# Kernel tuning notes

Hardware: AMD Instinct MI355X
Metric: run time of the kernel (lower is better)

## Reference

```python
import jax, jax.numpy as jnp
import numpy as np

MODES1 = 20
MODES2 = 20
WIDTH = 64
NUM_LAYERS = 4
B, H, W = 8, 256, 256


def _conv2d(x, w, b, pad):
    # x: (B,C,H,W), w: (O,I,kh,kw)
    y = jax.lax.conv_general_dilated(
        x, w, window_strides=(1, 1), padding=[(pad, pad), (pad, pad)],
        dimension_numbers=('NCHW', 'OIHW', 'NCHW'))
    return y + b[None, :, None, None]


def _spectral_conv(x, w1, w2, m1, m2):
    # x: (B,C,H,W); w1,w2: (I,O,m1,m2,2) real/imag pairs
    h, w = x.shape[-2], x.shape[-1]
    x_ft = jnp.fft.rfft2(x, norm='ortho')              # (B,C,H,W//2+1) complex
    w1c = w1[..., 0] + 1j * w1[..., 1]
    w2c = w2[..., 0] + 1j * w2[..., 1]
    top = jnp.einsum('bixy,ioxy->boxy', x_ft[:, :, :m1, :m2], w1c)
    bot = jnp.einsum('bixy,ioxy->boxy', x_ft[:, :, -m1:, :m2], w2c)
    out_ft = jnp.zeros((x.shape[0], w1.shape[1], h, w // 2 + 1), dtype=x_ft.dtype)
    out_ft = out_ft.at[:, :, :m1, :m2].set(top)
    out_ft = out_ft.at[:, :, -m1:, :m2].set(bot)
    return jnp.fft.irfft2(out_ft, s=(h, w), norm='ortho')


def setup_inputs() -> dict:
    key = jax.random.key(0)
    ks = jax.random.split(key, 16)
    C = WIDTH
    L = NUM_LAYERS
    scale = 1.0 / (C * C)
    inp = {
        'x': jax.random.normal(ks[0], (B, H, W, 3), dtype=jnp.float32),
        'fc0_w': jax.random.normal(ks[1], (3, C), dtype=jnp.float32) * 0.1,
        'fc0_b': jnp.zeros((C,), dtype=jnp.float32),
        'w1': scale * jax.random.uniform(ks[2], (L, C, C, MODES1, MODES2, 2), dtype=jnp.float32),
        'w2': scale * jax.random.uniform(ks[3], (L, C, C, MODES1, MODES2, 2), dtype=jnp.float32),
        'convh_w': jax.random.normal(ks[4], (L, C, C, 3, 3), dtype=jnp.float32) * 0.02,
        'convh_b': jnp.zeros((L, C), dtype=jnp.float32),
        'convw_w': jax.random.normal(ks[5], (L, C, C, 3, 3), dtype=jnp.float32) * 0.02,
        'convw_b': jnp.zeros((L, C), dtype=jnp.float32),
        'pw_w': jax.random.normal(ks[6], (L, C, C, 1, 1), dtype=jnp.float32) * 0.05,
        'pw_b': jnp.zeros((L, C), dtype=jnp.float32),
        'fc1_w': jax.random.normal(ks[7], (C, 128), dtype=jnp.float32) * 0.05,
        'fc1_b': jnp.zeros((128,), dtype=jnp.float32),
        'fc2_w': jax.random.normal(ks[8], (128, 1), dtype=jnp.float32) * 0.05,
        'fc2_b': jnp.zeros((1,), dtype=jnp.float32),
    }
    return inp


def reference(x, fc0_w, fc0_b, w1, w2, convh_w, convh_b, convw_w, convw_b,
              pw_w, pw_b, fc1_w, fc1_b, fc2_w, fc2_b):
    # fc0 lift: (B,H,W,3) -> (B,H,W,C) -> (B,C,H,W)
    h = jnp.einsum('bhwc,cd->bhwd', x, fc0_w) + fc0_b
    h = jnp.transpose(h, (0, 3, 1, 2))
    for i in range(NUM_LAYERS):
        x1 = _spectral_conv(h, w1[i], w2[i], MODES1, MODES2)
        # Mamba fallback block: two 3x3 convs summed (LayerNorm unused in forward)
        x2 = _conv2d(h, convh_w[i], convh_b[i], 1) + _conv2d(h, convw_w[i], convw_b[i], 1)
        x3 = _conv2d(h, pw_w[i], pw_b[i], 0)
        h = x1 + x2 + x3
        if i < NUM_LAYERS - 1:
            h = jax.nn.gelu(h, approximate=False)
    h = jnp.transpose(h, (0, 2, 3, 1))                  # (B,H,W,C)
    h = jnp.einsum('bhwc,cd->bhwd', h, fc1_w) + fc1_b
    h = jax.nn.gelu(h, approximate=False)
    out = jnp.einsum('bhwc,cd->bhwd', h, fc2_w) + fc2_b  # (B,H,W,1)
    return out
```

## Files before the change

kernel.cpp:

```cpp
#include <hip/hip_runtime.h>
#include <math.h>

#define NB 8
#define NC 64
#define NH 256
#define NW 256
#define NM 40
#define NKX 20
#define NL 4

typedef _Float16 f16x8 __attribute__((ext_vector_type(8)));
typedef float    f32x4 __attribute__((ext_vector_type(4)));

#define PERCB_FLOATS ((size_t)(2*4194304 + 655360 + 2*102400))
#define FIXED_FLOATS ((size_t)(6553600 + 10240 + 20480 + 147456 + 256 + 155648))

static __device__ __forceinline__ float gelu_f(float v) {
  return 0.5f * v * (1.f + erff(v * 0.70710678118654752f));
}
static __device__ __forceinline__ unsigned pack2(_Float16 a, _Float16 b) {
  union { _Float16 h[2]; unsigned u; } x; x.h[0] = a; x.h[1] = b; return x.u;
}

__global__ __launch_bounds__(256) void k_tables(float2* __restrict__ Tx,
                                                float2* __restrict__ Ty) {
  int t = blockIdx.x * 256 + threadIdx.x;
  const float w = (float)(2.0 * 3.14159265358979323846 / 256.0);
  if (t < NKX * 256) {
    int kx = t >> 8, x = t & 255;
    float th = (float)((kx * x) & 255) * w;
    Tx[t] = make_float2(cosf(th), sinf(th));
  }
  int u = t - NKX * 256;
  if (u >= 0 && u < NM * 256) {
    int m = u >> 8, y = u & 255;
    int ky = (m < 20) ? m : (m + 216);
    float th = (float)((ky * y) & 255) * w;
    Ty[u] = make_float2(cosf(th), sinf(th));
  }
}

__global__ __launch_bounds__(256) void k_wc(const float* __restrict__ ch,
                                            const float* __restrict__ cw,
                                            const float* __restrict__ pw,
                                            const float* __restrict__ chb,
                                            const float* __restrict__ cwb,
                                            const float* __restrict__ pwb,
                                            float* __restrict__ wc,
                                            float* __restrict__ bc) {
  int t = blockIdx.x * 256 + threadIdx.x;
  if (t < NL * NC * NC * 9) {
    int tap = t % 9;
    int io  = t / 9;
    int o   = io % 64;
    int i   = (io / 64) % 64;
    int l   = io / 4096;
    int src = ((l * 64 + o) * 64 + i) * 9 + tap;
    float v = ch[src] + cw[src];
    if (tap == 4) v += pw[(l * 64 + o) * 64 + i];
    wc[t] = v;
  }
  if (t < NL * NC) bc[t] = chb[t] + cwb[t] + pwb[t];
}

__global__ __launch_bounds__(256) void k_wpack(const float* __restrict__ wc,
                                               _Float16* __restrict__ whi,
                                               _Float16* __restrict__ wlo) {
  int t = blockIdx.x * 256 + threadIdx.x;
  int lane = t & 63;
  int nt   = (t >> 6) & 3;
  int chunk = (t >> 8) % 18;
  int l4   = t / 4608;
  int tap = chunk >> 1, half = chunk & 1;
  int o = nt * 16 + (lane & 15);
  _Float16 hi[8], lo[8];
  #pragma unroll
  for (int j = 0; j < 8; ++j) {
    int i = half * 32 + ((lane >> 4) << 3) + j;
    float v = wc[((l4 * 64 + i) * 64 + o) * 9 + tap];
    _Float16 h = (_Float16)v;
    hi[j] = h;
    lo[j] = (_Float16)(v - (float)h);
  }
  *(f16x8*)(whi + (size_t)t * 8) = *(f16x8*)hi;
  *(f16x8*)(wlo + (size_t)t * 8) = *(f16x8*)lo;
}

__global__ __launch_bounds__(256) void k_hpack(const float* __restrict__ w1,
                                               _Float16* __restrict__ whi,
                                               _Float16* __restrict__ wlo) {
  int t = blockIdx.x * 256 + threadIdx.x;
  int lane = t & 63;
  int nt   = (t >> 6) & 7;
  int chunk = t >> 9;
  int jo = nt * 16 + (lane & 15);
  _Float16 hi[8], lo[8];
  #pragma unroll
  for (int j = 0; j < 8; ++j) {
    int c = chunk * 32 + ((lane >> 4) << 3) + j;
    float v = w1[c * 128 + jo];
    _Float16 h = (_Float16)v;
    hi[j] = h;
    lo[j] = (_Float16)(v - (float)h);
  }
  *(f16x8*)(whi + (size_t)t * 8) = *(f16x8*)hi;
  *(f16x8*)(wlo + (size_t)t * 8) = *(f16x8*)lo;
}

__global__ __launch_bounds__(256) void k_fc0(const float* __restrict__ x,
                                             const float* __restrict__ w,
                                             const float* __restrict__ b,
                                             float* __restrict__ h, int b0) {
  int t = blockIdx.x * 256 + threadIdx.x;
  int ch = t & 63;
  int px = t >> 6;
  const float* xp = x + ((size_t)b0 * 65536 + px) * 3;
  h[t] = xp[0] * w[ch] + xp[1] * w[64 + ch] + xp[2] * w[128 + ch] + b[ch];
}

__global__ __launch_bounds__(256) void k_fwdx(const float* __restrict__ h,
                                              const float2* __restrict__ Tx,
                                              float2* __restrict__ Fx) {
  __shared__ float sm[16384];
  int bidx = blockIdx.x;
  int y  = bidx & 255;
  int bb = bidx >> 8;
  const float* hp = h + ((size_t)bb * 65536 + y * 256) * 64;
  for (int e = threadIdx.x; e < 4096; e += 256)
    *(float4*)(sm + e * 4) = *(const float4*)(hp + e * 4);
  __syncthreads();
  int w  = threadIdx.x >> 6;
  int ch = threadIdx.x & 63;
  float ar[5] = {0,0,0,0,0}, ai[5] = {0,0,0,0,0};
  #pragma unroll 4
  for (int x = 0; x < 256; x += 2) {
    float v0 = sm[x * 64 + ch];
    float v1 = sm[x * 64 + 64 + ch];
    #pragma unroll
    for (int q = 0; q < 5; ++q) {
      int kx = w * 5 + q;
      float4 t4 = *(const float4*)(Tx + kx * 256 + x);
      ar[q] += v0 * t4.x + v1 * t4.z;
      ai[q] -= v0 * t4.y + v1 * t4.w;
    }
  }
  float2* fp = Fx + ((size_t)(bb * 64 + ch) * 256 + y) * 20;
  #pragma unroll
  for (int q = 0; q < 5; ++q) fp[w * 5 + q] = make_float2(ar[q], ai[q]);
}

__global__ __launch_bounds__(256) void k_fwdy(const float2* __restrict__ Fx,
                                              const float2* __restrict__ Ty,
                                              float2* __restrict__ FxyT, int nbc) {
  __shared__ float2 sFx[5120];
  int bc = blockIdx.x;
  const float4* src = (const float4*)(Fx + (size_t)bc * 5120);
  float4* dst = (float4*)sFx;
  for (int e = threadIdx.x; e < 2560; e += 256) dst[e] = src[e];
  __syncthreads();
  for (int mk = threadIdx.x; mk < 800; mk += 256) {
    int kx = mk % 20, m = mk / 20;
    const float2* tp = Ty + m * 256;
    float re = 0.f, im = 0.f;
    #pragma unroll 4
    for (int yy = 0; yy < 256; ++yy) {
      float2 f = sFx[yy * 20 + kx];
      float2 wv = tp[yy];
      re += f.x * wv.x + f.y * wv.y;
      im += f.y * wv.x - f.x * wv.y;
    }
    FxyT[(size_t)mk * nbc + bc] = make_float2(re * (1.f / 256.f), im * (1.f / 256.f));
  }
}

__global__ __launch_bounds__(256) void k_wT(const float* __restrict__ w1,
                                            const float* __restrict__ w2,
                                            float2* __restrict__ wT, int l) {
  __shared__ float2 tile[32][33];
  int mk0 = blockIdx.x * 32;
  int io0 = blockIdx.y * 32;
  int tx = threadIdx.x & 31, ty0 = threadIdx.x >> 5;
  #pragma unroll
  for (int s = 0; s < 4; ++s) {
    int ty = ty0 * 4 + s;
    int mk = mk0 + tx, io = io0 + ty;
    int m = mk / 20, kx = mk % 20;
    const float* src = (m < 20) ? w1 : w2;
    int mm = (m < 20) ? m : (m - 20);
    size_t idx = ((((size_t)l * 4096 + io) * 20 + mm) * 20 + kx) * 2;
    tile[ty][tx] = make_float2(src[idx], src[idx + 1]);
  }
  __syncthreads();
  #pragma unroll
  for (int s = 0; s < 4; ++s) {
    int ty = ty0 * 4 + s;
    wT[(size_t)(mk0 + ty) * 4096 + (io0 + tx)] = tile[tx][ty];
  }
}

__global__ __launch_bounds__(256) void k_mix(const float2* __restrict__ FxyT,
                                             const float2* __restrict__ wT,
                                             float2* __restrict__ G, int nrows) {
  __shared__ float2 sf[512];
  int mk = blockIdx.x;
  for (int t = threadIdx.x; t < nrows; t += 256)
    sf[t] = FxyT[(size_t)mk * nrows + t];
  __syncthreads();
  const float2* wp = wT + (size_t)mk * 4096;
  for (int t = threadIdx.x; t < nrows; t += 256) {
    int b = t >> 6, o = t & 63;
    const float2* fb = sf + b * 64;
    float re = 0.f, im = 0.f;
    #pragma unroll 8
    for (int i = 0; i < 64; ++i) {
      float2 f = fb[i];
      float2 w = wp[i * 64 + o];
      re += f.x * w.x - f.y * w.y;
      im += f.x * w.y + f.y * w.x;
    }
    G[(size_t)(b * 64 + o) * 800 + mk] = make_float2(re, im);
  }
}

__global__ __launch_bounds__(256) void k_invy(const float2* __restrict__ G,
                                              const float2* __restrict__ Ty,
                                              float2* __restrict__ Gy) {
  int t  = blockIdx.x * 256 + threadIdx.x;
  int kx = t % 20;
  int y  = (t / 20) & 255;
  int bc = t / 5120;
  const float2* gp = G + (size_t)bc * 800 + kx;
  float re = 0.f, im = 0.f;
  #pragma unroll 4
  for (int m = 0; m < 40; ++m) {
    float2 g = gp[m * 20];
    float2 w = Ty[m * 256 + y];
    re += g.x * w.x - g.y * w.y;
    im += g.x * w.y + g.y * w.x;
  }
  Gy[t] = make_float2(re, im);
}

__global__ __launch_bounds__(256, 3) void k_conv(const float* __restrict__ hin,
                                                 const f16x8* __restrict__ wph,
                                                 const f16x8* __restrict__ wpl,
                                                 const float* __restrict__ bcb,
                                                 const float2* __restrict__ Gy,
                                                 const float2* __restrict__ Tx,
                                                 float* __restrict__ hout,
                                                 int dogelu) {
  __shared__ unsigned sAu[13056];
  int bidx = blockIdx.x;
  int xt = bidx & 7;
  int yt = (bidx >> 3) & 63;
  int bb = bidx >> 9;
  int x0 = xt << 5, y0 = yt << 2;
  int tid = threadIdx.x;
  int w = tid >> 6, lane = tid & 63, quad = lane >> 4, l15 = lane & 15;

  for (int e = tid; e < 204 * 32; e += 256) {
    int px = e >> 5, chp = e & 31;
    int rg = px / 34, cg = px % 34;
    int gy = y0 - 1 + rg, gx = x0 - 1 + cg;
    float2 v = make_float2(0.f, 0.f);
    if (gy >= 0 && gy < 256 && gx >= 0 && gx < 256)
      v = *(const float2*)(hin + (((size_t)bb * 256 + gy) * 256 + gx) * 64 + chp * 2);
    _Float16 h0 = (_Float16)v.x, h1 = (_Float16)v.y;
    _Float16 l0 = (_Float16)(v.x - (float)h0), l1 = (_Float16)(v.y - (float)h1);
    int dw = (px << 5) + (chp ^ ((px & 7) << 2));
    sAu[dw] = pack2(h0, h1);
    sAu[6528 + dw] = pack2(l0, l1);
  }
  __syncthreads();

  f32x4 acc[2][4];
  #pragma unroll
  for (int s = 0; s < 2; ++s)
    #pragma unroll
    for (int nt = 0; nt < 4; ++nt) acc[s][nt] = (f32x4){0.f, 0.f, 0.f, 0.f};

  #pragma unroll 1
  for (int tap = 0; tap < 9; ++tap) {
    int dy = tap / 3, dx = tap % 3;
    #pragma unroll
    for (int half = 0; half < 2; ++half) {
      int chunk = tap * 2 + half;
      const f16x8* bh = wph + (size_t)(chunk * 4) * 64 + lane;
      const f16x8* bl = wpl + (size_t)(chunk * 4) * 64 + lane;
      f16x8 bfh[4], bfl[4];
      #pragma unroll
      for (int nt = 0; nt < 4; ++nt) { bfh[nt] = bh[nt * 64]; bfl[nt] = bl[nt * 64]; }
      f16x8 afh[2], afl[2];
      #pragma unroll
      for (int s = 0; s < 2; ++s) {
        int px = (w + dy) * 34 + (s * 16 + dx) + l15;
        int dw = (px << 5) + (((half << 4) + (quad << 2)) ^ ((px & 7) << 2));
        afh[s] = *(const f16x8*)(sAu + dw);
        afl[s] = *(const f16x8*)(sAu + 6528 + dw);
      }
      #pragma unroll
      for (int s = 0; s < 2; ++s)
        #pragma unroll
        for (int nt = 0; nt < 4; ++nt) {
          acc[s][nt] = __builtin_amdgcn_mfma_f32_16x16x32_f16(afh[s], bfh[nt], acc[s][nt], 0, 0, 0);
          acc[s][nt] = __builtin_amdgcn_mfma_f32_16x16x32_f16(afh[s], bfl[nt], acc[s][nt], 0, 0, 0);
          acc[s][nt] = __builtin_amdgcn_mfma_f32_16x16x32_f16(afl[s], bfh[nt], acc[s][nt], 0, 0, 0);
        }
    }
  }

  __syncthreads();
  float2* sT  = (float2*)sAu;
  float2* sGy = (float2*)(sAu + 1280);
  float*  sTr = (float*)(sAu + 6528);
  for (int e = tid; e < 640; e += 256) {
    int kx = e >> 5, col = e & 31;
    sT[e] = Tx[kx * 256 + x0 + col];
  }
  const float scale = 1.f / 256.f;
  #pragma unroll 1
  for (int oh = 0; oh < 2; ++oh) {
    __syncthreads();
    for (int e = tid; e < 2560; e += 256) {
      int ol = e / 80, rem = e % 80;
      int row = rem / 20, kx = rem % 20;
      sGy[ol * 82 + row * 20 + kx] =
          Gy[((size_t)(bb * 64 + oh * 32 + ol) * 256 + (y0 + row)) * 20 + kx];
    }
    __syncthreads();
    #pragma unroll
    for (int nt2 = 0; nt2 < 2; ++nt2) {
      int nt = oh * 2 + nt2;
      int ol = nt2 * 16 + l15;
      int o  = oh * 32 + ol;
      float bias = bcb[o];
      const float2* gp = sGy + ol * 82 + w * 20;
      #pragma unroll
      for (int s = 0; s < 2; ++s) {
        int colb = s * 16 + (quad << 2);
        f32x4 sr = {0.f, 0.f, 0.f, 0.f};
        #pragma unroll
        for (int p = 0; p < 10; ++p) {
          float4 g = *(const float4*)(gp + 2 * p);
          float f0 = (p == 0) ? 1.f : 2.f;
          float4 tA = *(const float4*)(sT + (2 * p) * 32 + colb);
          float4 tB = *(const float4*)(sT + (2 * p) * 32 + colb + 2);
          sr.x += f0 * (g.x * tA.x - g.y * tA.y);
          sr.y += f0 * (g.x * tA.z - g.y * tA.w);
          sr.z += f0 * (g.x * tB.x - g.y * tB.y);
          sr.w += f0 * (g.x * tB.z - g.y * tB.w);
          float4 tC = *(const float4*)(sT + (2 * p + 1) * 32 + colb);
          float4 tD = *(const float4*)(sT + (2 * p + 1) * 32 + colb + 2);
          sr.x += 2.f * (g.z * tC.x - g.w * tC.y);
          sr.y += 2.f * (g.z * tC.z - g.w * tC.w);
          sr.z += 2.f * (g.z * tD.x - g.w * tD.y);
          sr.w += 2.f * (g.z * tD.z - g.w * tD.w);
        }
        #pragma unroll
        for (int r = 0; r < 4; ++r) {
          float v = acc[s][nt][r] + bias + sr[r] * scale;
          if (dogelu) v = gelu_f(v);
          sTr[(w * 32 + s * 16 + (quad << 2) + r) * 36 + ol] = v;
        }
      }
    }
    __syncthreads();
    #pragma unroll
    for (int k = 0; k < 4; ++k) {
      int e = tid + k * 256;
      int P = e >> 3, sub = e & 7;
      float4 v4 = *(const float4*)(sTr + P * 36 + sub * 4);
      int row = P >> 5, px32 = P & 31;
      *(float4*)(hout + (((size_t)bb * 256 + (y0 + row)) * 256 + x0 + px32) * 64
                 + oh * 32 + sub * 4) = v4;
    }
  }
}

__global__ __launch_bounds__(256, 2) void k_head(const float* __restrict__ h,
                                                 const f16x8* __restrict__ whi,
                                                 const f16x8* __restrict__ wlo,
                                                 const float* __restrict__ b1,
                                                 const float* __restrict__ w2,
                                                 const float* __restrict__ b2,
                                                 float* __restrict__ out, int b0) {
  int tid = threadIdx.x;
  int w = tid >> 6, lane = tid & 63, quad = lane >> 4, l15 = lane & 15;
  int px0 = blockIdx.x * 64 + w * 16;

  f32x4 acc[8];
  #pragma unroll
  for (int nt = 0; nt < 8; ++nt) acc[nt] = (f32x4){0.f, 0.f, 0.f, 0.f};

  #pragma unroll
  for (int half = 0; half < 2; ++half) {
    const float* ap = h + (size_t)(px0 + l15) * 64 + half * 32 + quad * 8;
    float4 a0 = *(const float4*)ap;
    float4 a1 = *(const float4*)(ap + 4);
    _Float16 ah[8], al[8];
    float av[8] = {a0.x, a0.y, a0.z, a0.w, a1.x, a1.y, a1.z, a1.w};
    #pragma unroll
    for (int j = 0; j < 8; ++j) {
      ah[j] = (_Float16)av[j];
      al[j] = (_Float16)(av[j] - (float)ah[j]);
    }
    f16x8 afh = *(f16x8*)ah, afl = *(f16x8*)al;
    #pragma unroll
    for (int nt = 0; nt < 8; ++nt) {
      f16x8 bh = whi[(size_t)(half * 8 + nt) * 64 + lane];
      f16x8 bl = wlo[(size_t)(half * 8 + nt) * 64 + lane];
      acc[nt] = __builtin_amdgcn_mfma_f32_16x16x32_f16(afh, bh, acc[nt], 0, 0, 0);
      acc[nt] = __builtin_amdgcn_mfma_f32_16x16x32_f16(afh, bl, acc[nt], 0, 0, 0);
      acc[nt] = __builtin_amdgcn_mfma_f32_16x16x32_f16(afl, bh, acc[nt], 0, 0, 0);
    }
  }

  float part[4] = {0.f, 0.f, 0.f, 0.f};
  #pragma unroll
  for (int nt = 0; nt < 8; ++nt) {
    int jo = nt * 16 + l15;
    float bb1 = b1[jo], ww2 = w2[jo];
    #pragma unroll
    for (int r = 0; r < 4; ++r)
      part[r] += gelu_f(acc[nt][r] + bb1) * ww2;
  }
  #pragma unroll
  for (int r = 0; r < 4; ++r) {
    float v = part[r];
    v += __shfl_xor(v, 1);
    v += __shfl_xor(v, 2);
    v += __shfl_xor(v, 4);
    v += __shfl_xor(v, 8);
    if (l15 == 0)
      out[(size_t)b0 * 65536 + px0 + quad * 4 + r] = v + b2[0];
  }
}

extern "C" void kernel_launch(void* const* d_in, const int* in_sizes, int n_in,
                              void* d_out, int out_size, void* d_ws, size_t ws_size,
                              hipStream_t stream) {
  const float* x    = (const float*)d_in[0];
  const float* fc0w = (const float*)d_in[1];
  const float* fc0b = (const float*)d_in[2];
  const float* w1   = (const float*)d_in[3];
  const float* w2   = (const float*)d_in[4];
  const float* chw  = (const float*)d_in[5];
  const float* chb  = (const float*)d_in[6];
  const float* cww  = (const float*)d_in[7];
  const float* cwb  = (const float*)d_in[8];
  const float* pww  = (const float*)d_in[9];
  const float* pwb  = (const float*)d_in[10];
  const float* fc1w = (const float*)d_in[11];
  const float* fc1b = (const float*)d_in[12];
  const float* fc2w = (const float*)d_in[13];
  const float* fc2b = (const float*)d_in[14];

  int cb = 1;
  for (int cand = 8; cand >= 1; cand >>= 1) {
    size_t need = (PERCB_FLOATS * (size_t)cand + FIXED_FLOATS) * sizeof(float);
    if (ws_size >= need) { cb = cand; break; }
  }

  const size_t szH = (size_t)cb * 4194304;

  float*  ws  = (float*)d_ws;
  float*  h   = ws;
  float*  h2  = h + szH;
  float2* Fx  = (float2*)(h2 + szH);
  float2* Fxy = (float2*)((float*)Fx + (size_t)cb * 655360);
  float2* G   = (float2*)((float*)Fxy + (size_t)cb * 102400);
  float2* wT  = (float2*)((float*)G + (size_t)cb * 102400);
  float2* Tx  = (float2*)((float*)wT + 6553600);
  float2* Ty  = (float2*)((float*)Tx + 10240);
  float*  wcb = (float*)Ty + 20480;
  float*  bcb = wcb + 147456;
  _Float16* wpkhi = (_Float16*)(bcb + 256);
  _Float16* wpklo = wpkhi + 147456;
  _Float16* w1hi  = wpklo + 147456;
  _Float16* w1lo  = w1hi + 8192;
  float2* Gy = Fx;

  k_tables<<<60, 256, 0, stream>>>(Tx, Ty);
  k_wc<<<576, 256, 0, stream>>>(chw, cww, pww, chb, cwb, pwb, wcb, bcb);
  k_wpack<<<72, 256, 0, stream>>>(wcb, wpkhi, wpklo);
  k_hpack<<<4, 256, 0, stream>>>(fc1w, w1hi, w1lo);

  for (int b0 = 0; b0 < NB; b0 += cb) {
    k_fc0<<<cb * 16384, 256, 0, stream>>>(x, fc0w, fc0b, h, b0);
    float* cur = h;
    float* nxt = h2;
    int nbc = cb * 64;
    for (int l = 0; l < NL; ++l) {
      k_fwdx<<<cb * 256, 256, 0, stream>>>(cur, Tx, Fx);
      k_fwdy<<<nbc, 256, 0, stream>>>(Fx, Ty, Fxy, nbc);
      k_wT<<<dim3(25, 128), 256, 0, stream>>>(w1, w2, wT, l);
      k_mix<<<NM * NKX, 256, 0, stream>>>(Fxy, wT, G, nbc);
      k_invy<<<cb * 1280, 256, 0, stream>>>(G, Ty, Gy);
      k_conv<<<cb * 512, 256, 0, stream>>>(cur,
                                           (const f16x8*)(wpkhi + (size_t)l * 36864),
                                           (const f16x8*)(wpklo + (size_t)l * 36864),
                                           bcb + (size_t)l * 64, Gy, Tx, nxt,
                                           (l < NL - 1) ? 1 : 0);
      float* tmp = cur; cur = nxt; nxt = tmp;
    }
    k_head<<<cb * 1024, 256, 0, stream>>>(cur, (const f16x8*)w1hi, (const f16x8*)w1lo,
                                          fc1b, fc2w, fc2b, (float*)d_out, b0);
  }
}
```

Measured before the change: 4.770 ms.

## Compute forward x-DFT with split-fp16 MFMA and simplify conv epilogue stores

The forward x-direction partial DFT is recast as a matrix multiply. Input rows are converted to hi/lo fp16 pairs in shared memory, and a prepacked fp16 twiddle matrix (built once by a new k_txpack kernel) feeds 16x16x32 MFMAs using three-product split precision. This replaces the scalar FMA loop over 256 x positions. The conv epilogue now loads all 64 output channels of Gy at once, hoists the bias loads, and writes results directly to global memory instead of transposing through shared memory in two halves. The direct stores are narrower and less coalesced, and the split-fp16 DFT may differ slightly in accuracy.

After: 4.374 ms. -8.3%, faster.

```diff
diff --git a/kernel.cpp b/kernel.cpp
--- a/kernel.cpp
+++ b/kernel.cpp
@@ -13,7 +13,7 @@
 typedef float    f32x4 __attribute__((ext_vector_type(4)));
 
 #define PERCB_FLOATS ((size_t)(2*4194304 + 655360 + 2*102400))
-#define FIXED_FLOATS ((size_t)(6553600 + 10240 + 20480 + 147456 + 256 + 155648))
+#define FIXED_FLOATS ((size_t)(6553600 + 10240 + 20480 + 147456 + 256 + 167936 + 2048))
 
 static __device__ __forceinline__ float gelu_f(float v) {
   return 0.5f * v * (1.f + erff(v * 0.70710678118654752f));
@@ -38,6 +38,26 @@
     float th = (float)((ky * y) & 255) * w;
     Ty[u] = make_float2(cosf(th), sinf(th));
   }
+}
+
+__global__ __launch_bounds__(256) void k_txpack(_Float16* __restrict__ th,
+                                                _Float16* __restrict__ tl) {
+  int t = blockIdx.x * 256 + threadIdx.x;
+  int j = t & 7, lane = (t >> 3) & 63;
+  int rest = t >> 9;
+  int nt = rest % 3, kc = rest / 3;
+  int x = kc * 32 + ((lane >> 4) << 3) + j;
+  int n = nt * 16 + (lane & 15);
+  float val = 0.f;
+  if (n < 40) {
+    int kx = n >> 1;
+    const float w = (float)(2.0 * 3.14159265358979323846 / 256.0);
+    float ang = (float)((kx * x) & 255) * w;
+    val = (n & 1) ? -sinf(ang) : cosf(ang);
+  }
+  _Float16 hi = (_Float16)val;
+  th[t] = hi;
+  tl[t] = (_Float16)(val - (float)hi);
 }
 
 __global__ __launch_bounds__(256) void k_wc(const float* __restrict__ ch,
@@ -119,34 +139,65 @@
 }
 
 __global__ __launch_bounds__(256) void k_fwdx(const float* __restrict__ h,
-                                              const float2* __restrict__ Tx,
+                                              const f16x8* __restrict__ txh,
+                                              const f16x8* __restrict__ txl,
                                               float2* __restrict__ Fx) {
-  __shared__ float sm[16384];
-  int bidx = blockIdx.x;
-  int y  = bidx & 255;
-  int bb = bidx >> 8;
-  const float* hp = h + ((size_t)bb * 65536 + y * 256) * 64;
-  for (int e = threadIdx.x; e < 4096; e += 256)
-    *(float4*)(sm + e * 4) = *(const float4*)(hp + e * 4);
-  __syncthreads();
-  int w  = threadIdx.x >> 6;
-  int ch = threadIdx.x & 63;
-  float ar[5] = {0,0,0,0,0}, ai[5] = {0,0,0,0,0};
-  #pragma unroll 4
-  for (int x = 0; x < 256; x += 2) {
-    float v0 = sm[x * 64 + ch];
-    float v1 = sm[x * 64 + 64 + ch];
-    #pragma unroll
-    for (int q = 0; q < 5; ++q) {
-      int kx = w * 5 + q;
-      float4 t4 = *(const float4*)(Tx + kx * 256 + x);
-      ar[q] += v0 * t4.x + v1 * t4.z;
-      ai[q] -= v0 * t4.y + v1 * t4.w;
-    }
-  }
-  float2* fp = Fx + ((size_t)(bb * 64 + ch) * 256 + y) * 20;
-  #pragma unroll
-  for (int q = 0; q < 5; ++q) fp[w * 5 + q] = make_float2(ar[q], ai[q]);
+  __shared__ _Float16 sH[64 * 136 * 2];
+  int y = blockIdx.x & 255, bb = blockIdx.x >> 8;
+  int tid = threadIdx.x;
+  int w = tid >> 6, lane = tid & 63, quad = lane >> 4, l15 = lane & 15;
+  const float* hp = h + ((size_t)(bb * 256 + y) * 256) * 64;
+
+  f32x4 acc[3];
+  #pragma unroll
+  for (int nt = 0; nt < 3; ++nt) acc[nt] = (f32x4){0.f, 0.f, 0.f, 0.f};
+
+  #pragma unroll 1
+  for (int hs = 0; hs < 2; ++hs) {
+    __syncthreads();
+    #pragma unroll
+    for (int it = 0; it < 8; ++it) {
+      int e = it * 256 + tid;
+      int xx = e >> 4;
+      int chg = (e & 15) << 2;
+      float4 v = *(const float4*)(hp + ((size_t)(hs * 128 + xx)) * 64 + chg);
+      float vv[4] = {v.x, v.y, v.z, v.w};
+      #pragma unroll
+      for (int k = 0; k < 4; ++k) {
+        _Float16 hi = (_Float16)vv[k];
+        sH[(chg + k) * 136 + xx] = hi;
+        sH[8704 + (chg + k) * 136 + xx] = (_Float16)(vv[k] - (float)hi);
+      }
+    }
+    __syncthreads();
+    #pragma unroll
+    for (int kc = 0; kc < 4; ++kc) {
+      int xb = kc * 32 + (quad << 3);
+      f16x8 ah = *(const f16x8*)(sH + (w * 16 + l15) * 136 + xb);
+      f16x8 al = *(const f16x8*)(sH + 8704 + (w * 16 + l15) * 136 + xb);
+      int kcg = hs * 4 + kc;
+      #pragma unroll
+      for (int nt = 0; nt < 3; ++nt) {
+        f16x8 bh = txh[(size_t)(kcg * 3 + nt) * 64 + lane];
+        f16x8 bl = txl[(size_t)(kcg * 3 + nt) * 64 + lane];
+        acc[nt] = __builtin_amdgcn_mfma_f32_16x16x32_f16(ah, bh, acc[nt], 0, 0, 0);
+        acc[nt] = __builtin_amdgcn_mfma_f32_16x16x32_f16(ah, bl, acc[nt], 0, 0, 0);
+        acc[nt] = __builtin_amdgcn_mfma_f32_16x16x32_f16(al, bh, acc[nt], 0, 0, 0);
+      }
+    }
+  }
+  #pragma unroll
+  for (int nt = 0; nt < 3; ++nt) {
+    int n = nt * 16 + l15;
+    if (n < 40) {
+      int kx = n >> 1, ri = n & 1;
+      #pragma unroll
+      for (int r = 0; r < 4; ++r) {
+        int c = w * 16 + (quad << 2) + r;
+        ((float*)(Fx + ((size_t)(bb * 64 + c) * 256 + y) * 20 + kx))[ri] = acc[nt][r];
+      }
+    }
+  }
 }
 
 __global__ __launch_bounds__(256) void k_fwdy(const float2* __restrict__ Fx,
@@ -258,6 +309,10 @@
   int tid = threadIdx.x;
   int w = tid >> 6, lane = tid & 63, quad = lane >> 4, l15 = lane & 15;
 
+  float bias[4];
+  #pragma unroll
+  for (int nt = 0; nt < 4; ++nt) bias[nt] = bcb[nt * 16 + l15];
+
   for (int e = tid; e < 204 * 32; e += 256) {
     int px = e >> 5, chp = e & 31;
     int rg = px / 34, cg = px % 34;
@@ -312,67 +367,58 @@
   __syncthreads();
   float2* sT  = (float2*)sAu;
   float2* sGy = (float2*)(sAu + 1280);
-  float*  sTr = (float*)(sAu + 6528);
   for (int e = tid; e < 640; e += 256) {
     int kx = e >> 5, col = e & 31;
     sT[e] = Tx[kx * 256 + x0 + col];
   }
+  for (int e = tid; e < 5120; e += 256) {
+    int o = e / 80, rem = e % 80;
+    int row = rem / 20, kx = rem % 20;
+    sGy[o * 82 + row * 20 + kx] =
+        Gy[((size_t)(bb * 64 + o) * 256 + (y0 + row)) * 20 + kx];
+  }
+  __syncthreads();
+
   const float scale = 1.f / 256.f;
-  #pragma unroll 1
-  for (int oh = 0; oh < 2; ++oh) {
-    __syncthreads();
-    for (int e = tid; e < 2560; e += 256) {
-      int ol = e / 80, rem = e % 80;
-      int row = rem / 20, kx = rem % 20;
-      sGy[ol * 82 + row * 20 + kx] =
-          Gy[((size_t)(bb * 64 + oh * 32 + ol) * 256 + (y0 + row)) * 20 + kx];
-    }
-    __syncthreads();
-    #pragma unroll
-    for (int nt2 = 0; nt2 < 2; ++nt2) {
-      int nt = oh * 2 + nt2;
-      int ol = nt2 * 16 + l15;
-      int o  = oh * 32 + ol;
-      float bias = bcb[o];
-      const float2* gp = sGy + ol * 82 + w * 20;
-      #pragma unroll
-      for (int s = 0; s < 2; ++s) {
-        int colb = s * 16 + (quad << 2);
-        f32x4 sr = {0.f, 0.f, 0.f, 0.f};
-        #pragma unroll
-        for (int p = 0; p < 10; ++p) {
-          float4 g = *(const float4*)(gp + 2 * p);
-          float f0 = (p == 0) ? 1.f : 2.f;
-          float4 tA = *(const float4*)(sT + (2 * p) * 32 + colb);
-          float4 tB = *(const float4*)(sT + (2 * p) * 32 + colb + 2);
-          sr.x += f0 * (g.x * tA.x - g.y * tA.y);
-          sr.y += f0 * (g.x * tA.z - g.y * tA.w);
-          sr.z += f0 * (g.x * tB.x - g.y * tB.y);
-          sr.w += f0 * (g.x * tB.z - g.y * tB.w);
-          float4 tC = *(const float4*)(sT + (2 * p + 1) * 32 + colb);
-          float4 tD = *(const float4*)(sT + (2 * p + 1) * 32 + colb + 2);
-          sr.x += 2.f * (g.z * tC.x - g.w * tC.y);
-          sr.y += 2.f * (g.z * tC.z - g.w * tC.w);
-          sr.z += 2.f * (g.z * tD.x - g.w * tD.y);
-          sr.w += 2.f * (g.z * tD.z - g.w * tD.w);
-        }
-        #pragma unroll
-        for (int r = 0; r < 4; ++r) {
-          float v = acc[s][nt][r] + bias + sr[r] * scale;
-          if (dogelu) v = gelu_f(v);
-          sTr[(w * 32 + s * 16 + (quad << 2) + r) * 36 + ol] = v;
-        }
+  #pragma unroll
+  for (int s = 0; s < 2; ++s) {
+    int colb = s * 16 + (quad << 2);
+    float vv[4][4];
+    #pragma unroll
+    for (int nt = 0; nt < 4; ++nt) {
+      int o = nt * 16 + l15;
+      const float2* gp = sGy + o * 82 + w * 20;
+      f32x4 sr = {0.f, 0.f, 0.f, 0.f};
+      #pragma unroll
+      for (int p = 0; p < 10; ++p) {
+        float4 g = *(const float4*)(gp + 2 * p);
+        float f0 = (p == 0) ? 1.f : 2.f;
+        float4 tA = *(const float4*)(sT + (2 * p) * 32 + colb);
+        float4 tB = *(const float4*)(sT + (2 * p) * 32 + colb + 2);
+        sr.x += f0 * (g.x * tA.x - g.y * tA.y);
+        sr.y += f0 * (g.x * tA.z - g.y * tA.w);
+        sr.z += f0 * (g.x * tB.x - g.y * tB.y);
+        sr.w += f0 * (g.x * tB.z - g.y * tB.w);
+        float4 tC = *(const float4*)(sT + (2 * p + 1) * 32 + colb);
+        float4 tD = *(const float4*)(sT + (2 * p + 1) * 32 + colb + 2);
+        sr.x += 2.f * (g.z * tC.x - g.w * tC.y);
+        sr.y += 2.f * (g.z * tC.z - g.w * tC.w);
+        sr.z += 2.f * (g.z * tD.x - g.w * tD.y);
+        sr.w += 2.f * (g.z * tD.z - g.w * tD.w);
       }
-    }
-    __syncthreads();
-    #pragma unroll
-    for (int k = 0; k < 4; ++k) {
-      int e = tid + k * 256;
-      int P = e >> 3, sub = e & 7;
-      float4 v4 = *(const float4*)(sTr + P * 36 + sub * 4);
-      int row = P >> 5, px32 = P & 31;
-      *(float4*)(hout + (((size_t)bb * 256 + (y0 + row)) * 256 + x0 + px32) * 64
-                 + oh * 32 + sub * 4) = v4;
+      #pragma unroll
+      for (int r = 0; r < 4; ++r) {
+        float v = acc[s][nt][r] + bias[nt] + sr[r] * scale;
+        if (dogelu) v = gelu_f(v);
+        vv[nt][r] = v;
+      }
+    }
+    #pragma unroll
+    for (int r = 0; r < 4; ++r) {
+      size_t base = (((size_t)bb * 256 + (y0 + w)) * 256 + x0 + colb + r) * 64;
+      #pragma unroll
+      for (int nt = 0; nt < 4; ++nt)
+        hout[base + nt * 16 + l15] = vv[nt][r];
     }
   }
 }
@@ -478,9 +524,12 @@
   _Float16* wpklo = wpkhi + 147456;
   _Float16* w1hi  = wpklo + 147456;
   _Float16* w1lo  = w1hi + 8192;
+  _Float16* txph  = w1lo + 8192;
+  _Float16* txpl  = txph + 12288;
   float2* Gy = Fx;
 
   k_tables<<<60, 256, 0, stream>>>(Tx, Ty);
+  k_txpack<<<48, 256, 0, stream>>>(txph, txpl);
   k_wc<<<576, 256, 0, stream>>>(chw, cww, pww, chb, cwb, pwb, wcb, bcb);
   k_wpack<<<72, 256, 0, stream>>>(wcb, wpkhi, wpklo);
   k_hpack<<<4, 256, 0, stream>>>(fc1w, w1hi, w1lo);
@@ -491,7 +540,8 @@
     float* nxt = h2;
     int nbc = cb * 64;
     for (int l = 0; l < NL; ++l) {
-      k_fwdx<<<cb * 256, 256, 0, stream>>>(cur, Tx, Fx);
+      k_fwdx<<<cb * 256, 256, 0, stream>>>(cur, (const f16x8*)txph,
+                                           (const f16x8*)txpl, Fx);
       k_fwdy<<<nbc, 256, 0, stream>>>(Fx, Ty, Fxy, nbc);
       k_wT<<<dim3(25, 128), 256, 0, stream>>>(w1, w2, wT, l);
       k_mix<<<NM * NKX, 256, 0, stream>>>(Fxy, wT, G, nbc);
```
